# Performance work log

Hardware: AMD Instinct MI355X
Metric: run time of the kernel (lower is better)

The kernel has to match this reference:

```python
import jax, jax.numpy as jnp
import numpy as np

D_MODEL = 1024
D_STATE = 16
D_CONV = 4
D_INNER = 2048  # expand * d_model
BATCH = 2
LENGTH = 2048


def silu(u):
    return u * jax.nn.sigmoid(u)


def setup_inputs() -> dict:
    key = jax.random.key(0)
    ks = jax.random.split(key, 8)
    sc = 0.02
    x = jax.random.normal(ks[0], (BATCH, LENGTH, D_MODEL), jnp.float32)
    W_in = jax.random.normal(ks[1], (2 * D_INNER, D_MODEL), jnp.float32) * sc
    conv_w = jax.random.normal(ks[2], (D_INNER, 1, D_CONV), jnp.float32) * 0.1
    conv_b = jnp.zeros((D_INNER,), jnp.float32)
    W_x = jax.random.normal(ks[3], (D_INNER + 2 * D_STATE, D_INNER), jnp.float32) * sc
    W_dt = jax.random.normal(ks[4], (D_INNER, D_INNER), jnp.float32) * sc
    b_dt = jnp.zeros((D_INNER,), jnp.float32)
    # A = arange(1, d_state+1) repeated for each inner channel (per source init)
    A_log = jnp.log(jnp.tile(jnp.arange(1, D_STATE + 1, dtype=jnp.float32), (D_INNER, 1)))
    D = jnp.ones((D_INNER,), jnp.float32)
    W_out = jax.random.normal(ks[5], (D_MODEL, D_INNER), jnp.float32) * sc
    ln_g = jnp.ones((D_MODEL,), jnp.float32)
    ln_b = jnp.zeros((D_MODEL,), jnp.float32)
    return dict(x=x, W_in=W_in, conv_w=conv_w, conv_b=conv_b, W_x=W_x, W_dt=W_dt,
                b_dt=b_dt, A_log=A_log, D=D, W_out=W_out, ln_g=ln_g, ln_b=ln_b)


def reference(x, W_in, conv_w, conv_b, W_x, W_dt, b_dt, A_log, D, W_out, ln_g, ln_b):
    b, l, _ = x.shape
    residual = x
    # in_proj, split into x-path and gate z
    xz = x @ W_in.T  # (b, l, 2*d_inner)
    xs, z = jnp.split(xz, 2, axis=-1)
    # depthwise causal conv1d (left pad d_conv-1, take first l outputs)
    xc = jnp.transpose(xs, (0, 2, 1))  # (b, d_inner, l)
    xc = jax.lax.conv_general_dilated(
        xc, conv_w, window_strides=(1,), padding=[(D_CONV - 1, 0)],
        dimension_numbers=('NCH', 'OIH', 'NCH'), feature_group_count=D_INNER)
    xc = xc + conv_b[None, :, None]
    u = silu(jnp.transpose(xc, (0, 2, 1)))  # (b, l, d_inner)
    # SSM parameter projection
    proj = u @ W_x.T  # (b, l, d_inner + 2*d_state)
    d_in, Bm, Cm = jnp.split(proj, [D_INNER, D_INNER + D_STATE], axis=-1)
    delta = jax.nn.softplus(d_in @ W_dt.T + b_dt)  # (b, l, d_inner)
    A = -jnp.exp(A_log)  # (d_inner, d_state)
    dA = jnp.exp(delta[..., None] * A)                         # (b, l, d, n)
    dBu = delta[..., None] * Bm[:, :, None, :] * u[..., None]  # (b, l, d, n)

    def step(state, inp):
        dA_t, dBu_t, c_t = inp
        state = state * dA_t + dBu_t            # (b, d, n)
        y_t = jnp.einsum('bdn,bn->bd', state, c_t)
        return state, y_t

    init = jnp.zeros((b, D_INNER, D_STATE), x.dtype)
    _, ys = jax.lax.scan(step, init, (jnp.transpose(dA, (1, 0, 2, 3)),
                                      jnp.transpose(dBu, (1, 0, 2, 3)),
                                      jnp.transpose(Cm, (1, 0, 2))))
    y = jnp.transpose(ys, (1, 0, 2)) + u * D  # (b, l, d_inner)
    y = y * silu(z)
    out = y @ W_out.T + residual
    mu = jnp.mean(out, axis=-1, keepdims=True)
    var = jnp.var(out, axis=-1, keepdims=True)
    return (out - mu) / jnp.sqrt(var + 1e-5) * ln_g + ln_b
```

## Files before the change

### kernel.cpp

```cpp
#include <hip/hip_runtime.h>

typedef unsigned short u16;
typedef unsigned int u32;
typedef __bf16 bf16x8_t __attribute__((ext_vector_type(8)));
typedef float f32x4_t __attribute__((ext_vector_type(4)));


#define NCH 64
#define CLEN 32

__device__ __forceinline__ u16 f2bf(float f) {
  u32 u = __float_as_uint(f);
  return (u16)((u + 0x7fffu + ((u >> 16) & 1u)) >> 16);
}
__device__ __forceinline__ float bf2f(u16 h) { return __uint_as_float(((u32)h) << 16); }

__device__ __forceinline__ void async_ld16(const u16* g, u16* l) {
  __builtin_amdgcn_global_load_lds((const __attribute__((address_space(1))) void*)g,
                                   (__attribute__((address_space(3))) void*)l, 16, 0, 0);
}

__global__ void k_prep(const float* __restrict__ x, u16* __restrict__ x_bf,
                       const float* __restrict__ W_in, u16* __restrict__ Win_bf,
                       const float* __restrict__ W_dt, u16* __restrict__ Wdt_bf,
                       const float* __restrict__ W_out, u16* __restrict__ Wout_bf,
                       const float* __restrict__ W_x, u16* __restrict__ WxT,
                       u16* __restrict__ Weff_ext) {
  __shared__ u16 tile[64][72];
  int blk = blockIdx.x;
  if (blk < 14592) {
    int g = blk * 256 + threadIdx.x;
    const float* src;
    u16* dst;
    int rel;
    bool rd = true;
    if (g < 1048576) { src = x; dst = x_bf; rel = g; }
    else if (g < 2097152) { src = W_in; dst = Win_bf; rel = g - 1048576; }
    else if (g < 3145728) { src = W_dt; dst = Wdt_bf; rel = g - 2097152; }
    else if (g < 3670016) { src = W_out; dst = Wout_bf; rel = g - 3145728; }
    else if (g < 3686400) { src = W_x + 4194304; dst = Weff_ext + (size_t)2048 * 2048; rel = g - 3670016; }
    else { dst = Weff_ext + (size_t)2080 * 2048; rel = g - 3686400; rd = false; src = x; }
    u32 lo = 0, hi = 0;
    if (rd) {
      float4 v = reinterpret_cast<const float4*>(src)[rel];
      lo = (u32)f2bf(v.x) | ((u32)f2bf(v.y) << 16);
      hi = (u32)f2bf(v.z) | ((u32)f2bf(v.w) << 16);
    }
    reinterpret_cast<uint2*>(dst)[rel] = make_uint2(lo, hi);
  } else {
    int bid = blk - 14592;
    int bx = bid & 31;
    int by = bid >> 5;
    int t = threadIdx.x;
#pragma unroll
    for (int i = 0; i < 4; ++i) {
      int idx = i * 256 + t;
      int r = idx >> 4;
      int c = (idx & 15) * 4;
      float4 v = *reinterpret_cast<const float4*>(W_x + (size_t)(by * 64 + r) * 2048 + bx * 64 + c);
      tile[r][c] = f2bf(v.x); tile[r][c + 1] = f2bf(v.y);
      tile[r][c + 2] = f2bf(v.z); tile[r][c + 3] = f2bf(v.w);
    }
    __syncthreads();
#pragma unroll
    for (int i = 0; i < 2; ++i) {
      int idx = i * 256 + t;
      int r = idx >> 3;
      int c = (idx & 7) * 8;
      u16 tmp[8];
#pragma unroll
      for (int e = 0; e < 8; ++e) tmp[e] = tile[c + e][r];
      *reinterpret_cast<uint4*>(WxT + (size_t)(bx * 64 + r) * 2048 + by * 64 + c) =
          *reinterpret_cast<uint4*>(tmp);
    }
  }
}

template <bool WB, bool WF>
__device__ __forceinline__ void gemm_tile(
    u16* sA, u16* sB, int bx, int by, int kbase,
    const u16* __restrict__ A, int lda, const u16* __restrict__ B, int ldb,
    float* __restrict__ Cf, int fcol0, int ldcf,
    u16* __restrict__ Cb, int ldc, int K) {
  const int tid = threadIdx.x;
  const int lane = tid & 63;
  const int wave = tid >> 6;
  const size_t tm = (size_t)by * 128;
  const size_t tn = (size_t)bx * 128;
  const int wm = (wave & 1) * 64;
  const int wn = (wave >> 1) * 64;
  const int mrow = lane & 15;
  const int quad = lane >> 4;

  f32x4_t acc[4][4];
#pragma unroll
  for (int i = 0; i < 4; ++i)
#pragma unroll
    for (int j = 0; j < 4; ++j) {
      acc[i][j][0] = 0.f; acc[i][j][1] = 0.f; acc[i][j][2] = 0.f; acc[i][j][3] = 0.f;
    }

  for (int k0 = 0; k0 < K; k0 += 64) {
#pragma unroll
    for (int j = 0; j < 4; ++j) {
      int idx = j * 256 + tid;
      int row = idx >> 3;
      int col = (idx & 7) << 3;
      async_ld16(A + (tm + row) * (size_t)lda + (kbase + k0 + col), sA + (size_t)idx * 8);
      async_ld16(B + (tn + row) * (size_t)ldb + (kbase + k0 + col), sB + (size_t)idx * 8);
    }
    __syncthreads();
#pragma unroll
    for (int kk = 0; kk < 64; kk += 32) {
      bf16x8_t af[4], bfr[4];
#pragma unroll
      for (int i = 0; i < 4; ++i)
        af[i] = *reinterpret_cast<const bf16x8_t*>(sA + (wm + i * 16 + mrow) * 64 + kk + quad * 8);
#pragma unroll
      for (int i = 0; i < 4; ++i)
        bfr[i] = *reinterpret_cast<const bf16x8_t*>(sB + (wn + i * 16 + mrow) * 64 + kk + quad * 8);
#pragma unroll
      for (int i = 0; i < 4; ++i)
#pragma unroll
        for (int j = 0; j < 4; ++j)
          acc[i][j] = __builtin_amdgcn_mfma_f32_16x16x32_bf16(af[i], bfr[j], acc[i][j], 0, 0, 0);
    }
    __syncthreads();
  }

#pragma unroll
  for (int i = 0; i < 4; ++i)
#pragma unroll
    for (int j = 0; j < 4; ++j) {
      size_t r0 = tm + wm + i * 16 + quad * 4;
      size_t c = tn + wn + j * 16 + mrow;
#pragma unroll
      for (int r = 0; r < 4; ++r) {
        float v = acc[i][j][r];
        if (WF && (int)c >= fcol0) Cf[(r0 + r) * (size_t)ldcf + (c - fcol0)] = v;
        if (WB && (int)c < fcol0) Cb[(r0 + r) * (size_t)ldc + c] = f2bf(v);
      }
    }
}

template <bool WB, bool WF>
__global__ __launch_bounds__(256, 2) void k_gemm(
    const u16* __restrict__ A, int lda, const u16* __restrict__ B, int ldb,
    float* __restrict__ Cf, int fcol0, int ldcf, size_t fsplit,
    u16* __restrict__ Cb, int ldc, int K) {
  __shared__ __align__(16) u16 sA[128 * 64];
  __shared__ __align__(16) u16 sB[128 * 64];
  gemm_tile<WB, WF>(sA, sB, blockIdx.x, blockIdx.y, blockIdx.z * K, A, lda, B, ldb,
                    Cf + (size_t)blockIdx.z * fsplit, fcol0, ldcf, Cb, ldc, K);
}

__global__ __launch_bounds__(256, 2) void k_gemm_dual(
    const u16* __restrict__ A1, const u16* __restrict__ B1, u16* __restrict__ C1,
    const u16* __restrict__ A2, const u16* __restrict__ B2, u16* __restrict__ C2) {
  __shared__ __align__(16) u16 sA[128 * 64];
  __shared__ __align__(16) u16 sB[128 * 64];
  int b = blockIdx.x;
  if (b < 1024) {
    gemm_tile<true, false>(sA, sB, b & 31, b >> 5, 0, A1, 1024, B1, 1024,
                           nullptr, 1 << 30, 0, C1, 4096, 1024);
  } else {
    int b2 = b - 1024;
    gemm_tile<true, false>(sA, sB, b2 & 15, b2 >> 4, 0, A2, 2048, B2, 2048,
                           nullptr, 1 << 30, 0, C2, 2048, 2048);
  }
}

__global__ void k_conv_silu(const u16* __restrict__ xz, const float* __restrict__ cw,
                            const float* __restrict__ cb, u16* __restrict__ u) {
  int bl = blockIdx.x;
  int l = bl & 2047;
  int d0 = threadIdx.x * 8;
  float acc[8];
  float4 cb0 = *reinterpret_cast<const float4*>(cb + d0);
  float4 cb1 = *reinterpret_cast<const float4*>(cb + d0 + 4);
  acc[0] = cb0.x; acc[1] = cb0.y; acc[2] = cb0.z; acc[3] = cb0.w;
  acc[4] = cb1.x; acc[5] = cb1.y; acc[6] = cb1.z; acc[7] = cb1.w;
  float4 w[8];
#pragma unroll
  for (int i = 0; i < 8; ++i) w[i] = *reinterpret_cast<const float4*>(cw + (d0 + i) * 4);
#pragma unroll
  for (int k = 0; k < 4; ++k) {
    int lp = l + k - 3;
    if (lp >= 0) {
      bf16x8_t xv = *reinterpret_cast<const bf16x8_t*>(xz + ((size_t)(bl + k - 3) << 12) + d0);
#pragma unroll
      for (int i = 0; i < 8; ++i)
        acc[i] += (float)xv[i] * reinterpret_cast<const float*>(&w[i])[k];
    }
  }
  u16 tmp[8];
#pragma unroll
  for (int i = 0; i < 8; ++i) {
    float s = acc[i] / (1.f + __expf(-acc[i]));
    tmp[i] = f2bf(s);
  }
  *reinterpret_cast<uint4*>(u + ((size_t)bl << 11) + d0) = *reinterpret_cast<uint4*>(tmp);
}

__device__ __forceinline__ float softplus_fast(float x) {
  return __logf(1.f + __expf(x));
}

__global__ void k_scan1(const u16* __restrict__ dpre, const float* __restrict__ bdt,
                        const u16* __restrict__ u, const float* __restrict__ projBC,
                        const float* __restrict__ A_log, float* __restrict__ sF,
                        float* __restrict__ aF) {
  int d = blockIdx.x * 256 + threadIdx.x;
  int c = blockIdx.y, b = blockIdx.z;
  float A[16], s[16], ap[16];
#pragma unroll
  for (int q = 0; q < 4; ++q) {
    float4 al = reinterpret_cast<const float4*>(A_log + d * 16)[q];
    A[q * 4 + 0] = -__expf(al.x); A[q * 4 + 1] = -__expf(al.y);
    A[q * 4 + 2] = -__expf(al.z); A[q * 4 + 3] = -__expf(al.w);
  }
#pragma unroll
  for (int n = 0; n < 16; ++n) { s[n] = 0.f; ap[n] = 1.f; }
  float bd = bdt[d];
  int t0 = c * CLEN;
  for (int t = t0; t < t0 + CLEN; ++t) {
    size_t rb = (size_t)(b * 2048 + t);
    float delta = softplus_fast(bf2f(dpre[rb * 2048 + d]) + bd);
    float du = delta * bf2f(u[rb * 2048 + d]);
    const float4* Bp = reinterpret_cast<const float4*>(projBC + rb * 128);
    float4 B0 = Bp[0], B1 = Bp[1], B2 = Bp[2], B3 = Bp[3];
    float Bv[16] = {B0.x, B0.y, B0.z, B0.w, B1.x, B1.y, B1.z, B1.w,
                    B2.x, B2.y, B2.z, B2.w, B3.x, B3.y, B3.z, B3.w};
#pragma unroll
    for (int n = 0; n < 16; ++n) {
      float dA = __expf(delta * A[n]);
      s[n] = fmaf(s[n], dA, du * Bv[n]);
      ap[n] *= dA;
    }
  }
  size_t o = ((size_t)((b * NCH + c) * 2048 + d)) << 4;
#pragma unroll
  for (int q = 0; q < 4; ++q) {
    reinterpret_cast<float4*>(sF + o)[q] = make_float4(s[q * 4], s[q * 4 + 1], s[q * 4 + 2], s[q * 4 + 3]);
    reinterpret_cast<float4*>(aF + o)[q] = make_float4(ap[q * 4], ap[q * 4 + 1], ap[q * 4 + 2], ap[q * 4 + 3]);
  }
}

__global__ void k_scan_carry(const float* __restrict__ sF, const float* __restrict__ aF,
                             float* __restrict__ carry) {
  int g = blockIdx.x * 256 + threadIdx.x;
  int b = g >> 15;
  int dn = g & 32767;
  float S = 0.f;
#pragma unroll 4
  for (int c = 0; c < NCH; ++c) {
    size_t idx = ((size_t)(b * NCH + c) << 15) + dn;
    carry[idx] = S;
    S = S * aF[idx] + sF[idx];
  }
}

__global__ void k_scan3(const u16* __restrict__ dpre, const float* __restrict__ bdt,
                        const u16* __restrict__ u, const float* __restrict__ projBC,
                        const float* __restrict__ A_log, const float* __restrict__ carry,
                        const float* __restrict__ Dvec, const u16* __restrict__ xz,
                        u16* __restrict__ ybf) {
  int d = blockIdx.x * 256 + threadIdx.x;
  int c = blockIdx.y, b = blockIdx.z;
  float A[16], s[16];
#pragma unroll
  for (int q = 0; q < 4; ++q) {
    float4 al = reinterpret_cast<const float4*>(A_log + d * 16)[q];
    A[q * 4 + 0] = -__expf(al.x); A[q * 4 + 1] = -__expf(al.y);
    A[q * 4 + 2] = -__expf(al.z); A[q * 4 + 3] = -__expf(al.w);
  }
  size_t o = ((size_t)((b * NCH + c) * 2048 + d)) << 4;
#pragma unroll
  for (int q = 0; q < 4; ++q) {
    float4 cv = reinterpret_cast<const float4*>(carry + o)[q];
    s[q * 4] = cv.x; s[q * 4 + 1] = cv.y; s[q * 4 + 2] = cv.z; s[q * 4 + 3] = cv.w;
  }
  float bd = bdt[d];
  float Dd = Dvec[d];
  int t0 = c * CLEN;
  for (int t = t0; t < t0 + CLEN; ++t) {
    size_t rb = (size_t)(b * 2048 + t);
    float delta = softplus_fast(bf2f(dpre[rb * 2048 + d]) + bd);
    float uv = bf2f(u[rb * 2048 + d]);
    float du = delta * uv;
    const float4* Bp = reinterpret_cast<const float4*>(projBC + rb * 128);
    float4 B0 = Bp[0], B1 = Bp[1], B2 = Bp[2], B3 = Bp[3];
    float4 C0 = Bp[4], C1 = Bp[5], C2 = Bp[6], C3 = Bp[7];
    float Bv[16] = {B0.x, B0.y, B0.z, B0.w, B1.x, B1.y, B1.z, B1.w,
                    B2.x, B2.y, B2.z, B2.w, B3.x, B3.y, B3.z, B3.w};
    float Cv[16] = {C0.x, C0.y, C0.z, C0.w, C1.x, C1.y, C1.z, C1.w,
                    C2.x, C2.y, C2.z, C2.w, C3.x, C3.y, C3.z, C3.w};
    float yv = 0.f;
#pragma unroll
    for (int n = 0; n < 16; ++n) {
      float dA = __expf(delta * A[n]);
      s[n] = fmaf(s[n], dA, du * Bv[n]);
      yv = fmaf(s[n], Cv[n], yv);
    }
    yv += uv * Dd;
    float z = bf2f(xz[(rb << 12) + 2048 + d]);
    yv *= z / (1.f + __expf(-z));
    ybf[rb * 2048 + d] = f2bf(yv);
  }
}

__global__ void k_ln(const float* __restrict__ pre, const float* __restrict__ x,
                     const float* __restrict__ gam, const float* __restrict__ bet,
                     float* __restrict__ out) {
  int row = blockIdx.x, tid = threadIdx.x;
  size_t base = (size_t)row * 1024 + tid * 4;
  float4 v = *reinterpret_cast<const float4*>(pre + base);
  float4 p1 = *reinterpret_cast<const float4*>(pre + 4194304 + base);
  float4 r = *reinterpret_cast<const float4*>(x + base);
  v.x += p1.x + r.x; v.y += p1.y + r.y; v.z += p1.z + r.z; v.w += p1.w + r.w;
  float s = v.x + v.y + v.z + v.w;
  float s2 = v.x * v.x + v.y * v.y + v.z * v.z + v.w * v.w;
#pragma unroll
  for (int o = 32; o >= 1; o >>= 1) {
    s += __shfl_xor(s, o);
    s2 += __shfl_xor(s2, o);
  }
  __shared__ float red[8];
  int lane = tid & 63, wv = tid >> 6;
  if (lane == 0) { red[wv] = s; red[4 + wv] = s2; }
  __syncthreads();
  s = red[0] + red[1] + red[2] + red[3];
  s2 = red[4] + red[5] + red[6] + red[7];
  float mu = s * (1.f / 1024.f);
  float var = s2 * (1.f / 1024.f) - mu * mu;
  float rstd = rsqrtf(var + 1e-5f);
  float4 gg = *reinterpret_cast<const float4*>(gam + tid * 4);
  float4 bb = *reinterpret_cast<const float4*>(bet + tid * 4);
  float4 o;
  o.x = (v.x - mu) * rstd * gg.x + bb.x;
  o.y = (v.y - mu) * rstd * gg.y + bb.y;
  o.z = (v.z - mu) * rstd * gg.z + bb.z;
  o.w = (v.w - mu) * rstd * gg.w + bb.w;
  *reinterpret_cast<float4*>(out + base) = o;
}

extern "C" void kernel_launch(void* const* d_in, const int* in_sizes, int n_in,
                              void* d_out, int out_size, void* d_ws, size_t ws_size,
                              hipStream_t stream) {
  (void)in_sizes; (void)n_in; (void)out_size; (void)ws_size;
  const float* x = (const float*)d_in[0];
  const float* W_in = (const float*)d_in[1];
  const float* conv_w = (const float*)d_in[2];
  const float* conv_b = (const float*)d_in[3];
  const float* W_x = (const float*)d_in[4];
  const float* W_dt = (const float*)d_in[5];
  const float* b_dt = (const float*)d_in[6];
  const float* A_log = (const float*)d_in[7];
  const float* Dv = (const float*)d_in[8];
  const float* W_out = (const float*)d_in[9];
  const float* ln_g = (const float*)d_in[10];
  const float* ln_b = (const float*)d_in[11];
  float* out = (float*)d_out;

  char* p = (char*)d_ws;
  u16* xz_bf = (u16*)p;      p += (size_t)4096 * 4096 * 2;
  u16* u_bf = (u16*)p;       p += (size_t)4096 * 2048 * 2;
  float* projBC = (float*)p; p += (size_t)4096 * 128 * 4;
  u16* dpre_bf = (u16*)p;    p += (size_t)4096 * 2048 * 2;
  u16* ybf = (u16*)p;        p += (size_t)4096 * 2048 * 2;
  float* sF = (float*)p;     p += (size_t)2 * NCH * 2048 * 16 * 4;
  float* aF = (float*)p;     p += (size_t)2 * NCH * 2048 * 16 * 4;
  float* carry = (float*)p;  p += (size_t)2 * NCH * 2048 * 16 * 4;
  u16* WxT_bf = (u16*)p;     p += (size_t)2048 * 2048 * 2;
  u16* Weff_ext = (u16*)p;   p += (size_t)2176 * 2048 * 2;
  u16* Wdt_bf = (u16*)p;     p += (size_t)2048 * 2048 * 2;
  u16* Wout_bf = (u16*)p;    p += (size_t)1024 * 2048 * 2;
  u16* x_bf = (u16*)p;       p += (size_t)4096 * 1024 * 2;
  u16* Win_bf = (u16*)p;     p += (size_t)4096 * 1024 * 2;
  float* outpre = sF;

  k_prep<<<15616, 256, 0, stream>>>(x, x_bf, W_in, Win_bf, W_dt, Wdt_bf, W_out, Wout_bf,
                                    W_x, WxT_bf, Weff_ext);
  k_gemm_dual<<<1280, 256, 0, stream>>>(x_bf, Win_bf, xz_bf, Wdt_bf, WxT_bf, Weff_ext);
  k_conv_silu<<<4096, 256, 0, stream>>>(xz_bf, conv_w, conv_b, u_bf);
  k_gemm<true, true><<<dim3(17, 32), 256, 0, stream>>>(
      u_bf, 2048, Weff_ext, 2048, projBC, 2048, 128, 0, dpre_bf, 2048, 2048);
  k_scan1<<<dim3(8, NCH, 2), 256, 0, stream>>>(dpre_bf, b_dt, u_bf, projBC, A_log, sF, aF);
  k_scan_carry<<<256, 256, 0, stream>>>(sF, aF, carry);
  k_scan3<<<dim3(8, NCH, 2), 256, 0, stream>>>(dpre_bf, b_dt, u_bf, projBC, A_log, carry,
                                               Dv, xz_bf, ybf);
  k_gemm<false, true><<<dim3(8, 32, 2), 256, 0, stream>>>(
      ybf, 2048, Wout_bf, 2048, outpre, 0, 1024, (size_t)4096 * 1024, nullptr, 0, 1024);
  k_ln<<<4096, 256, 0, stream>>>(outpre, x, ln_g, ln_b, out);
}
```

Measured before the change: 433.2 us.

## Fuse all phases into one persistent cooperative kernel with grid syncs

Replaces the nine separate kernel launches with a single cooperative persistent kernel of 512 blocks. Each phase loops over its work units and a grid-wide barrier separates consecutive phases. The aim is to remove launch overhead and inter-kernel gaps. In exchange, each phase is capped at 512 resident blocks, which limits occupancy for the memory-bound phases. The grid syncs add their own cost, and the GEMM tile counts (1280, 544) do not divide evenly into 512 blocks, leaving a tail. If the cooperative launch fails, the code falls back to separate launches.

After: 1.009 ms. +133.0%, slower.

```diff
diff --git a/kernel.cpp b/kernel.cpp
--- a/kernel.cpp
+++ b/kernel.cpp
@@ -1,4 +1,7 @@
 #include <hip/hip_runtime.h>
+#include <hip/hip_cooperative_groups.h>
+
+namespace cg = cooperative_groups;
 
 typedef unsigned short u16;
 typedef unsigned int u32;
@@ -8,6 +11,7 @@
 
 #define NCH 64
 #define CLEN 32
+#define GRID 512
 
 __device__ __forceinline__ u16 f2bf(float f) {
   u32 u = __float_as_uint(f);
@@ -20,26 +24,27 @@
                                    (__attribute__((address_space(3))) void*)l, 16, 0, 0);
 }
 
-__global__ void k_prep(const float* __restrict__ x, u16* __restrict__ x_bf,
-                       const float* __restrict__ W_in, u16* __restrict__ Win_bf,
-                       const float* __restrict__ W_dt, u16* __restrict__ Wdt_bf,
-                       const float* __restrict__ W_out, u16* __restrict__ Wout_bf,
-                       const float* __restrict__ W_x, u16* __restrict__ WxT,
-                       u16* __restrict__ Weff_ext) {
-  __shared__ u16 tile[64][72];
-  int blk = blockIdx.x;
+struct P {
+  const float *x, *W_in, *conv_w, *conv_b, *W_x, *W_dt, *b_dt, *A_log, *Dv, *W_out,
+      *ln_g, *ln_b;
+  float* out;
+  u16 *x_bf, *Win_bf, *Wdt_bf, *Wout_bf, *WxT, *Weff_ext, *xz_bf, *u_bf, *dpre_bf, *ybf;
+  float *projBC, *sF, *aF, *carry, *outpre;
+};
+
+__device__ void ph_prep(const P& p, int blk, u16* smem) {
   if (blk < 14592) {
     int g = blk * 256 + threadIdx.x;
     const float* src;
     u16* dst;
     int rel;
     bool rd = true;
-    if (g < 1048576) { src = x; dst = x_bf; rel = g; }
-    else if (g < 2097152) { src = W_in; dst = Win_bf; rel = g - 1048576; }
-    else if (g < 3145728) { src = W_dt; dst = Wdt_bf; rel = g - 2097152; }
-    else if (g < 3670016) { src = W_out; dst = Wout_bf; rel = g - 3145728; }
-    else if (g < 3686400) { src = W_x + 4194304; dst = Weff_ext + (size_t)2048 * 2048; rel = g - 3670016; }
-    else { dst = Weff_ext + (size_t)2080 * 2048; rel = g - 3686400; rd = false; src = x; }
+    if (g < 1048576) { src = p.x; dst = p.x_bf; rel = g; }
+    else if (g < 2097152) { src = p.W_in; dst = p.Win_bf; rel = g - 1048576; }
+    else if (g < 3145728) { src = p.W_dt; dst = p.Wdt_bf; rel = g - 2097152; }
+    else if (g < 3670016) { src = p.W_out; dst = p.Wout_bf; rel = g - 3145728; }
+    else if (g < 3686400) { src = p.W_x + 4194304; dst = p.Weff_ext + (size_t)2048 * 2048; rel = g - 3670016; }
+    else { dst = p.Weff_ext + (size_t)2080 * 2048; rel = g - 3686400; rd = false; src = p.x; }
     u32 lo = 0, hi = 0;
     if (rd) {
       float4 v = reinterpret_cast<const float4*>(src)[rel];
@@ -48,6 +53,7 @@
     }
     reinterpret_cast<uint2*>(dst)[rel] = make_uint2(lo, hi);
   } else {
+    u16(*tile)[72] = reinterpret_cast<u16(*)[72]>(smem);
     int bid = blk - 14592;
     int bx = bid & 31;
     int by = bid >> 5;
@@ -57,7 +63,7 @@
       int idx = i * 256 + t;
       int r = idx >> 4;
       int c = (idx & 15) * 4;
-      float4 v = *reinterpret_cast<const float4*>(W_x + (size_t)(by * 64 + r) * 2048 + bx * 64 + c);
+      float4 v = *reinterpret_cast<const float4*>(p.W_x + (size_t)(by * 64 + r) * 2048 + bx * 64 + c);
       tile[r][c] = f2bf(v.x); tile[r][c + 1] = f2bf(v.y);
       tile[r][c + 2] = f2bf(v.z); tile[r][c + 3] = f2bf(v.w);
     }
@@ -70,9 +76,10 @@
       u16 tmp[8];
 #pragma unroll
       for (int e = 0; e < 8; ++e) tmp[e] = tile[c + e][r];
-      *reinterpret_cast<uint4*>(WxT + (size_t)(bx * 64 + r) * 2048 + by * 64 + c) =
+      *reinterpret_cast<uint4*>(p.WxT + (size_t)(bx * 64 + r) * 2048 + by * 64 + c) =
           *reinterpret_cast<uint4*>(tmp);
     }
+    __syncthreads();
   }
 }
 
@@ -143,51 +150,33 @@
     }
 }
 
-template <bool WB, bool WF>
-__global__ __launch_bounds__(256, 2) void k_gemm(
-    const u16* __restrict__ A, int lda, const u16* __restrict__ B, int ldb,
-    float* __restrict__ Cf, int fcol0, int ldcf, size_t fsplit,
-    u16* __restrict__ Cb, int ldc, int K) {
-  __shared__ __align__(16) u16 sA[128 * 64];
-  __shared__ __align__(16) u16 sB[128 * 64];
-  gemm_tile<WB, WF>(sA, sB, blockIdx.x, blockIdx.y, blockIdx.z * K, A, lda, B, ldb,
-                    Cf + (size_t)blockIdx.z * fsplit, fcol0, ldcf, Cb, ldc, K);
-}
-
-__global__ __launch_bounds__(256, 2) void k_gemm_dual(
-    const u16* __restrict__ A1, const u16* __restrict__ B1, u16* __restrict__ C1,
-    const u16* __restrict__ A2, const u16* __restrict__ B2, u16* __restrict__ C2) {
-  __shared__ __align__(16) u16 sA[128 * 64];
-  __shared__ __align__(16) u16 sB[128 * 64];
-  int b = blockIdx.x;
-  if (b < 1024) {
-    gemm_tile<true, false>(sA, sB, b & 31, b >> 5, 0, A1, 1024, B1, 1024,
-                           nullptr, 1 << 30, 0, C1, 4096, 1024);
+__device__ void ph_dual(const P& p, int blk, u16* sA, u16* sB) {
+  if (blk < 1024) {
+    gemm_tile<true, false>(sA, sB, blk & 31, blk >> 5, 0, p.x_bf, 1024, p.Win_bf, 1024,
+                           nullptr, 1 << 30, 0, p.xz_bf, 4096, 1024);
   } else {
-    int b2 = b - 1024;
-    gemm_tile<true, false>(sA, sB, b2 & 15, b2 >> 4, 0, A2, 2048, B2, 2048,
-                           nullptr, 1 << 30, 0, C2, 2048, 2048);
-  }
-}
-
-__global__ void k_conv_silu(const u16* __restrict__ xz, const float* __restrict__ cw,
-                            const float* __restrict__ cb, u16* __restrict__ u) {
-  int bl = blockIdx.x;
+    int b2 = blk - 1024;
+    gemm_tile<true, false>(sA, sB, b2 & 15, b2 >> 4, 0, p.Wdt_bf, 2048, p.WxT, 2048,
+                           nullptr, 1 << 30, 0, p.Weff_ext, 2048, 2048);
+  }
+}
+
+__device__ void ph_conv(const P& p, int bl) {
   int l = bl & 2047;
   int d0 = threadIdx.x * 8;
   float acc[8];
-  float4 cb0 = *reinterpret_cast<const float4*>(cb + d0);
-  float4 cb1 = *reinterpret_cast<const float4*>(cb + d0 + 4);
+  float4 cb0 = *reinterpret_cast<const float4*>(p.conv_b + d0);
+  float4 cb1 = *reinterpret_cast<const float4*>(p.conv_b + d0 + 4);
   acc[0] = cb0.x; acc[1] = cb0.y; acc[2] = cb0.z; acc[3] = cb0.w;
   acc[4] = cb1.x; acc[5] = cb1.y; acc[6] = cb1.z; acc[7] = cb1.w;
   float4 w[8];
 #pragma unroll
-  for (int i = 0; i < 8; ++i) w[i] = *reinterpret_cast<const float4*>(cw + (d0 + i) * 4);
+  for (int i = 0; i < 8; ++i) w[i] = *reinterpret_cast<const float4*>(p.conv_w + (d0 + i) * 4);
 #pragma unroll
   for (int k = 0; k < 4; ++k) {
     int lp = l + k - 3;
     if (lp >= 0) {
-      bf16x8_t xv = *reinterpret_cast<const bf16x8_t*>(xz + ((size_t)(bl + k - 3) << 12) + d0);
+      bf16x8_t xv = *reinterpret_cast<const bf16x8_t*>(p.xz_bf + ((size_t)(bl + k - 3) << 12) + d0);
 #pragma unroll
       for (int i = 0; i < 8; ++i)
         acc[i] += (float)xv[i] * reinterpret_cast<const float*>(&w[i])[k];
@@ -199,35 +188,38 @@
     float s = acc[i] / (1.f + __expf(-acc[i]));
     tmp[i] = f2bf(s);
   }
-  *reinterpret_cast<uint4*>(u + ((size_t)bl << 11) + d0) = *reinterpret_cast<uint4*>(tmp);
+  *reinterpret_cast<uint4*>(p.u_bf + ((size_t)bl << 11) + d0) = *reinterpret_cast<uint4*>(tmp);
+}
+
+__device__ void ph_gemm2(const P& p, int blk, u16* sA, u16* sB) {
+  int bx = blk % 17, by = blk / 17;
+  gemm_tile<true, true>(sA, sB, bx, by, 0, p.u_bf, 2048, p.Weff_ext, 2048,
+                        p.projBC, 2048, 128, p.dpre_bf, 2048, 2048);
 }
 
 __device__ __forceinline__ float softplus_fast(float x) {
   return __logf(1.f + __expf(x));
 }
 
-__global__ void k_scan1(const u16* __restrict__ dpre, const float* __restrict__ bdt,
-                        const u16* __restrict__ u, const float* __restrict__ projBC,
-                        const float* __restrict__ A_log, float* __restrict__ sF,
-                        float* __restrict__ aF) {
-  int d = blockIdx.x * 256 + threadIdx.x;
-  int c = blockIdx.y, b = blockIdx.z;
+__device__ void ph_scan1(const P& p, int unit) {
+  int xb = unit & 7, c = (unit >> 3) & 63, b = unit >> 9;
+  int d = xb * 256 + threadIdx.x;
   float A[16], s[16], ap[16];
 #pragma unroll
   for (int q = 0; q < 4; ++q) {
-    float4 al = reinterpret_cast<const float4*>(A_log + d * 16)[q];
+    float4 al = reinterpret_cast<const float4*>(p.A_log + d * 16)[q];
     A[q * 4 + 0] = -__expf(al.x); A[q * 4 + 1] = -__expf(al.y);
     A[q * 4 + 2] = -__expf(al.z); A[q * 4 + 3] = -__expf(al.w);
   }
 #pragma unroll
   for (int n = 0; n < 16; ++n) { s[n] = 0.f; ap[n] = 1.f; }
-  float bd = bdt[d];
+  float bd = p.b_dt[d];
   int t0 = c * CLEN;
   for (int t = t0; t < t0 + CLEN; ++t) {
     size_t rb = (size_t)(b * 2048 + t);
-    float delta = softplus_fast(bf2f(dpre[rb * 2048 + d]) + bd);
-    float du = delta * bf2f(u[rb * 2048 + d]);
-    const float4* Bp = reinterpret_cast<const float4*>(projBC + rb * 128);
+    float delta = softplus_fast(bf2f(p.dpre_bf[rb * 2048 + d]) + bd);
+    float du = delta * bf2f(p.u_bf[rb * 2048 + d]);
+    const float4* Bp = reinterpret_cast<const float4*>(p.projBC + rb * 128);
     float4 B0 = Bp[0], B1 = Bp[1], B2 = Bp[2], B3 = Bp[3];
     float Bv[16] = {B0.x, B0.y, B0.z, B0.w, B1.x, B1.y, B1.z, B1.w,
                     B2.x, B2.y, B2.z, B2.w, B3.x, B3.y, B3.z, B3.w};
@@ -241,54 +233,48 @@
   size_t o = ((size_t)((b * NCH + c) * 2048 + d)) << 4;
 #pragma unroll
   for (int q = 0; q < 4; ++q) {
-    reinterpret_cast<float4*>(sF + o)[q] = make_float4(s[q * 4], s[q * 4 + 1], s[q * 4 + 2], s[q * 4 + 3]);
-    reinterpret_cast<float4*>(aF + o)[q] = make_float4(ap[q * 4], ap[q * 4 + 1], ap[q * 4 + 2], ap[q * 4 + 3]);
-  }
-}
-
-__global__ void k_scan_carry(const float* __restrict__ sF, const float* __restrict__ aF,
-                             float* __restrict__ carry) {
-  int g = blockIdx.x * 256 + threadIdx.x;
+    reinterpret_cast<float4*>(p.sF + o)[q] = make_float4(s[q * 4], s[q * 4 + 1], s[q * 4 + 2], s[q * 4 + 3]);
+    reinterpret_cast<float4*>(p.aF + o)[q] = make_float4(ap[q * 4], ap[q * 4 + 1], ap[q * 4 + 2], ap[q * 4 + 3]);
+  }
+}
+
+__device__ void ph_carry(const P& p, int g) {
   int b = g >> 15;
   int dn = g & 32767;
   float S = 0.f;
 #pragma unroll 4
   for (int c = 0; c < NCH; ++c) {
     size_t idx = ((size_t)(b * NCH + c) << 15) + dn;
-    carry[idx] = S;
-    S = S * aF[idx] + sF[idx];
-  }
-}
-
-__global__ void k_scan3(const u16* __restrict__ dpre, const float* __restrict__ bdt,
-                        const u16* __restrict__ u, const float* __restrict__ projBC,
-                        const float* __restrict__ A_log, const float* __restrict__ carry,
-                        const float* __restrict__ Dvec, const u16* __restrict__ xz,
-                        u16* __restrict__ ybf) {
-  int d = blockIdx.x * 256 + threadIdx.x;
-  int c = blockIdx.y, b = blockIdx.z;
+    p.carry[idx] = S;
+    S = S * p.aF[idx] + p.sF[idx];
+  }
+}
+
+__device__ void ph_scan3(const P& p, int unit) {
+  int xb = unit & 7, c = (unit >> 3) & 63, b = unit >> 9;
+  int d = xb * 256 + threadIdx.x;
   float A[16], s[16];
 #pragma unroll
   for (int q = 0; q < 4; ++q) {
-    float4 al = reinterpret_cast<const float4*>(A_log + d * 16)[q];
+    float4 al = reinterpret_cast<const float4*>(p.A_log + d * 16)[q];
     A[q * 4 + 0] = -__expf(al.x); A[q * 4 + 1] = -__expf(al.y);
     A[q * 4 + 2] = -__expf(al.z); A[q * 4 + 3] = -__expf(al.w);
   }
   size_t o = ((size_t)((b * NCH + c) * 2048 + d)) << 4;
 #pragma unroll
   for (int q = 0; q < 4; ++q) {
-    float4 cv = reinterpret_cast<const float4*>(carry + o)[q];
+    float4 cv = reinterpret_cast<const float4*>(p.carry + o)[q];
     s[q * 4] = cv.x; s[q * 4 + 1] = cv.y; s[q * 4 + 2] = cv.z; s[q * 4 + 3] = cv.w;
   }
-  float bd = bdt[d];
-  float Dd = Dvec[d];
+  float bd = p.b_dt[d];
+  float Dd = p.Dv[d];
   int t0 = c * CLEN;
   for (int t = t0; t < t0 + CLEN; ++t) {
     size_t rb = (size_t)(b * 2048 + t);
-    float delta = softplus_fast(bf2f(dpre[rb * 2048 + d]) + bd);
-    float uv = bf2f(u[rb * 2048 + d]);
+    float delta = softplus_fast(bf2f(p.dpre_bf[rb * 2048 + d]) + bd);
+    float uv = bf2f(p.u_bf[rb * 2048 + d]);
     float du = delta * uv;
-    const float4* Bp = reinterpret_cast<const float4*>(projBC + rb * 128);
+    const float4* Bp = reinterpret_cast<const float4*>(p.projBC + rb * 128);
     float4 B0 = Bp[0], B1 = Bp[1], B2 = Bp[2], B3 = Bp[3];
     float4 C0 = Bp[4], C1 = Bp[5], C2 = Bp[6], C3 = Bp[7];
     float Bv[16] = {B0.x, B0.y, B0.z, B0.w, B1.x, B1.y, B1.z, B1.w,
@@ -303,20 +289,24 @@
       yv = fmaf(s[n], Cv[n], yv);
     }
     yv += uv * Dd;
-    float z = bf2f(xz[(rb << 12) + 2048 + d]);
+    float z = bf2f(p.xz_bf[(rb << 12) + 2048 + d]);
     yv *= z / (1.f + __expf(-z));
-    ybf[rb * 2048 + d] = f2bf(yv);
-  }
-}
-
-__global__ void k_ln(const float* __restrict__ pre, const float* __restrict__ x,
-                     const float* __restrict__ gam, const float* __restrict__ bet,
-                     float* __restrict__ out) {
-  int row = blockIdx.x, tid = threadIdx.x;
+    p.ybf[rb * 2048 + d] = f2bf(yv);
+  }
+}
+
+__device__ void ph_gemm4(const P& p, int blk, u16* sA, u16* sB) {
+  int bx = blk & 7, by = (blk >> 3) & 31, z = blk >> 8;
+  gemm_tile<false, true>(sA, sB, bx, by, z * 1024, p.ybf, 2048, p.Wout_bf, 2048,
+                         p.outpre + (size_t)z * 4194304, 0, 1024, nullptr, 0, 1024);
+}
+
+__device__ void ph_ln(const P& p, int row, float* red) {
+  int tid = threadIdx.x;
   size_t base = (size_t)row * 1024 + tid * 4;
-  float4 v = *reinterpret_cast<const float4*>(pre + base);
-  float4 p1 = *reinterpret_cast<const float4*>(pre + 4194304 + base);
-  float4 r = *reinterpret_cast<const float4*>(x + base);
+  float4 v = *reinterpret_cast<const float4*>(p.outpre + base);
+  float4 p1 = *reinterpret_cast<const float4*>(p.outpre + 4194304 + base);
+  float4 r = *reinterpret_cast<const float4*>(p.x + base);
   v.x += p1.x + r.x; v.y += p1.y + r.y; v.z += p1.z + r.z; v.w += p1.w + r.w;
   float s = v.x + v.y + v.z + v.w;
   float s2 = v.x * v.x + v.y * v.y + v.z * v.z + v.w * v.w;
@@ -325,7 +315,6 @@
     s += __shfl_xor(s, o);
     s2 += __shfl_xor(s2, o);
   }
-  __shared__ float red[8];
   int lane = tid & 63, wv = tid >> 6;
   if (lane == 0) { red[wv] = s; red[4 + wv] = s2; }
   __syncthreads();
@@ -334,62 +323,118 @@
   float mu = s * (1.f / 1024.f);
   float var = s2 * (1.f / 1024.f) - mu * mu;
   float rstd = rsqrtf(var + 1e-5f);
-  float4 gg = *reinterpret_cast<const float4*>(gam + tid * 4);
-  float4 bb = *reinterpret_cast<const float4*>(bet + tid * 4);
+  float4 gg = *reinterpret_cast<const float4*>(p.ln_g + tid * 4);
+  float4 bb = *reinterpret_cast<const float4*>(p.ln_b + tid * 4);
   float4 o;
   o.x = (v.x - mu) * rstd * gg.x + bb.x;
   o.y = (v.y - mu) * rstd * gg.y + bb.y;
   o.z = (v.z - mu) * rstd * gg.z + bb.z;
   o.w = (v.w - mu) * rstd * gg.w + bb.w;
-  *reinterpret_cast<float4*>(out + base) = o;
+  *reinterpret_cast<float4*>(p.out + base) = o;
+  __syncthreads();
+}
+
+__global__ __launch_bounds__(256, 2) void k_mega(P p) {
+  __shared__ __align__(16) u16 smem[2 * 128 * 64];
+  u16* sA = smem;
+  u16* sB = smem + 8192;
+  cg::grid_group grid = cg::this_grid();
+  const int bid = blockIdx.x;
+  const int tid = threadIdx.x;
+
+  for (int blk = bid; blk < 15616; blk += GRID) ph_prep(p, blk, smem);
+  grid.sync();
+  for (int blk = bid; blk < 1280; blk += GRID) ph_dual(p, blk, sA, sB);
+  grid.sync();
+  for (int bl = bid; bl < 4096; bl += GRID) ph_conv(p, bl);
+  grid.sync();
+  for (int blk = bid; blk < 544; blk += GRID) ph_gemm2(p, blk, sA, sB);
+  grid.sync();
+  for (int u = bid; u < 1024; u += GRID) ph_scan1(p, u);
+  grid.sync();
+  for (int g = bid * 256 + tid; g < 65536; g += GRID * 256) ph_carry(p, g);
+  grid.sync();
+  for (int u = bid; u < 1024; u += GRID) ph_scan3(p, u);
+  grid.sync();
+  for (int blk = bid; blk < 512; blk += GRID) ph_gemm4(p, blk, sA, sB);
+  grid.sync();
+  for (int row = bid; row < 4096; row += GRID) ph_ln(p, row, (float*)smem);
+}
+
+__global__ void k_phase_prep(P p) {
+  __shared__ __align__(16) u16 smem[64 * 72];
+  ph_prep(p, blockIdx.x, smem);
+}
+__global__ __launch_bounds__(256, 2) void k_phase_dual(P p) {
+  __shared__ __align__(16) u16 smem[2 * 128 * 64];
+  ph_dual(p, blockIdx.x, smem, smem + 8192);
+}
+__global__ void k_phase_conv(P p) { ph_conv(p, blockIdx.x); }
+__global__ __launch_bounds__(256, 2) void k_phase_gemm2(P p) {
+  __shared__ __align__(16) u16 smem[2 * 128 * 64];
+  ph_gemm2(p, blockIdx.x, smem, smem + 8192);
+}
+__global__ void k_phase_scan1(P p) { ph_scan1(p, blockIdx.x); }
+__global__ void k_phase_carry(P p) { ph_carry(p, blockIdx.x * 256 + threadIdx.x); }
+__global__ void k_phase_scan3(P p) { ph_scan3(p, blockIdx.x); }
+__global__ __launch_bounds__(256, 2) void k_phase_gemm4(P p) {
+  __shared__ __align__(16) u16 smem[2 * 128 * 64];
+  ph_gemm4(p, blockIdx.x, smem, smem + 8192);
+}
+__global__ void k_phase_ln(P p) {
+  __shared__ float red[8];
+  ph_ln(p, blockIdx.x, red);
 }
 
 extern "C" void kernel_launch(void* const* d_in, const int* in_sizes, int n_in,
                               void* d_out, int out_size, void* d_ws, size_t ws_size,
                               hipStream_t stream) {
   (void)in_sizes; (void)n_in; (void)out_size; (void)ws_size;
-  const float* x = (const float*)d_in[0];
-  const float* W_in = (const float*)d_in[1];
-  const float* conv_w = (const float*)d_in[2];
-  const float* conv_b = (const float*)d_in[3];
-  const float* W_x = (const float*)d_in[4];
-  const float* W_dt = (const float*)d_in[5];
-  const float* b_dt = (const float*)d_in[6];
-  const float* A_log = (const float*)d_in[7];
-  const float* Dv = (const float*)d_in[8];
-  const float* W_out = (const float*)d_in[9];
-  const float* ln_g = (const float*)d_in[10];
-  const float* ln_b = (const float*)d_in[11];
-  float* out = (float*)d_out;
+
+  P prm;
+  prm.x = (const float*)d_in[0];
+  prm.W_in = (const float*)d_in[1];
+  prm.conv_w = (const float*)d_in[2];
+  prm.conv_b = (const float*)d_in[3];
+  prm.W_x = (const float*)d_in[4];
+  prm.W_dt = (const float*)d_in[5];
+  prm.b_dt = (const float*)d_in[6];
+  prm.A_log = (const float*)d_in[7];
+  prm.Dv = (const float*)d_in[8];
+  prm.W_out = (const float*)d_in[9];
+  prm.ln_g = (const float*)d_in[10];
+  prm.ln_b = (const float*)d_in[11];
+  prm.out = (float*)d_out;
 
   char* p = (char*)d_ws;
-  u16* xz_bf = (u16*)p;      p += (size_t)4096 * 4096 * 2;
-  u16* u_bf = (u16*)p;       p += (size_t)4096 * 2048 * 2;
-  float* projBC = (float*)p; p += (size_t)4096 * 128 * 4;
-  u16* dpre_bf = (u16*)p;    p += (size_t)4096 * 2048 * 2;
-  u16* ybf = (u16*)p;        p += (size_t)4096 * 2048 * 2;
-  float* sF = (float*)p;     p += (size_t)2 * NCH * 2048 * 16 * 4;
-  float* aF = (float*)p;     p += (size_t)2 * NCH * 2048 * 16 * 4;
-  float* carry = (float*)p;  p += (size_t)2 * NCH * 2048 * 16 * 4;
-  u16* WxT_bf = (u16*)p;     p += (size_t)2048 * 2048 * 2;
-  u16* Weff_ext = (u16*)p;   p += (size_t)2176 * 2048 * 2;
-  u16* Wdt_bf = (u16*)p;     p += (size_t)2048 * 2048 * 2;
-  u16* Wout_bf = (u16*)p;    p += (size_t)1024 * 2048 * 2;
-  u16* x_bf = (u16*)p;       p += (size_t)4096 * 1024 * 2;
-  u16* Win_bf = (u16*)p;     p += (size_t)4096 * 1024 * 2;
-  float* outpre = sF;
-
-  k_prep<<<15616, 256, 0, stream>>>(x, x_bf, W_in, Win_bf, W_dt, Wdt_bf, W_out, Wout_bf,
-                                    W_x, WxT_bf, Weff_ext);
-  k_gemm_dual<<<1280, 256, 0, stream>>>(x_bf, Win_bf, xz_bf, Wdt_bf, WxT_bf, Weff_ext);
-  k_conv_silu<<<4096, 256, 0, stream>>>(xz_bf, conv_w, conv_b, u_bf);
-  k_gemm<true, true><<<dim3(17, 32), 256, 0, stream>>>(
-      u_bf, 2048, Weff_ext, 2048, projBC, 2048, 128, 0, dpre_bf, 2048, 2048);
-  k_scan1<<<dim3(8, NCH, 2), 256, 0, stream>>>(dpre_bf, b_dt, u_bf, projBC, A_log, sF, aF);
-  k_scan_carry<<<256, 256, 0, stream>>>(sF, aF, carry);
-  k_scan3<<<dim3(8, NCH, 2), 256, 0, stream>>>(dpre_bf, b_dt, u_bf, projBC, A_log, carry,
-                                               Dv, xz_bf, ybf);
-  k_gemm<false, true><<<dim3(8, 32, 2), 256, 0, stream>>>(
-      ybf, 2048, Wout_bf, 2048, outpre, 0, 1024, (size_t)4096 * 1024, nullptr, 0, 1024);
-  k_ln<<<4096, 256, 0, stream>>>(outpre, x, ln_g, ln_b, out);
-}
+  prm.xz_bf = (u16*)p;    p += (size_t)4096 * 4096 * 2;
+  prm.u_bf = (u16*)p;     p += (size_t)4096 * 2048 * 2;
+  prm.projBC = (float*)p; p += (size_t)4096 * 128 * 4;
+  prm.dpre_bf = (u16*)p;  p += (size_t)4096 * 2048 * 2;
+  prm.ybf = (u16*)p;      p += (size_t)4096 * 2048 * 2;
+  prm.sF = (float*)p;     p += (size_t)2 * NCH * 2048 * 16 * 4;
+  prm.aF = (float*)p;     p += (size_t)2 * NCH * 2048 * 16 * 4;
+  prm.carry = (float*)p;  p += (size_t)2 * NCH * 2048 * 16 * 4;
+  prm.WxT = (u16*)p;      p += (size_t)2048 * 2048 * 2;
+  prm.Weff_ext = (u16*)p; p += (size_t)2176 * 2048 * 2;
+  prm.Wdt_bf = (u16*)p;   p += (size_t)2048 * 2048 * 2;
+  prm.Wout_bf = (u16*)p;  p += (size_t)1024 * 2048 * 2;
+  prm.x_bf = (u16*)p;     p += (size_t)4096 * 1024 * 2;
+  prm.Win_bf = (u16*)p;   p += (size_t)4096 * 1024 * 2;
+  prm.outpre = prm.sF;
+
+  void* args[] = {&prm};
+  hipError_t e = hipLaunchCooperativeKernel((const void*)k_mega, dim3(GRID), dim3(256),
+                                            args, 0, stream);
+  if (e != hipSuccess) {
+    k_phase_prep<<<15616, 256, 0, stream>>>(prm);
+    k_phase_dual<<<1280, 256, 0, stream>>>(prm);
+    k_phase_conv<<<4096, 256, 0, stream>>>(prm);
+    k_phase_gemm2<<<544, 256, 0, stream>>>(prm);
+    k_phase_scan1<<<1024, 256, 0, stream>>>(prm);
+    k_phase_carry<<<256, 256, 0, stream>>>(prm);
+    k_phase_scan3<<<1024, 256, 0, stream>>>(prm);
+    k_phase_gemm4<<<512, 256, 0, stream>>>(prm);
+    k_phase_ln<<<4096, 256, 0, stream>>>(prm);
+  }
+}
```
